# Kernel optimization log

Measured on AMD Instinct MI355X. Metric: run time of the kernel, lower is better.

## Reference

```python
import math
import jax, jax.numpy as jnp
import numpy as np

B, T, N, D = 8, 12, 512, 64
NN = 16           # neighbors per node
S_FACTOR = 5      # self.s
D_HEAD = 64       # self.d (scaling)
M_SAMPLES = int(S_FACTOR * math.log2(N))  # 45


def _ln(x):
    # LayerNorm over last dim, no affine (elementwise_affine=False)
    mu = jnp.mean(x, axis=-1, keepdims=True)
    var = jnp.var(x, axis=-1, keepdims=True)
    return (x - mu) / jnp.sqrt(var + 1e-5)


def setup_inputs() -> dict:
    key = jax.random.key(0)
    ks = jax.random.split(key, 16)
    w = lambda k, shp: jax.random.normal(k, shp, dtype=jnp.float32) * 0.05
    inp = {
        "x": jax.random.normal(ks[0], (B, T, N, D), dtype=jnp.float32),
        "adj": jax.random.randint(ks[1], (N, NN), 0, N),
        "eigvec": jax.random.normal(ks[2], (D, N, 1), dtype=jnp.float32),
        "eigvalue": jax.random.normal(ks[3], (D,), dtype=jnp.float32),
        "Wq": w(ks[4], (D, D)), "bq": jnp.zeros((D,), jnp.float32),
        "Wk": w(ks[5], (D, D)), "bk": jnp.zeros((D,), jnp.float32),
        "Wv": w(ks[6], (D, D)), "bv": jnp.zeros((D,), jnp.float32),
        "Wo": w(ks[7], (D, D)), "bo": jnp.zeros((D,), jnp.float32),
        "Wp": w(ks[8], (D, 1)), "bp": jnp.zeros((1,), jnp.float32),
        "W1": w(ks[9], (D, D)), "b1": jnp.zeros((D,), jnp.float32),
        "W2": w(ks[10], (D, D)), "b2": jnp.zeros((D,), jnp.float32),
    }
    return inp


def reference(x, adj, eigvec, eigvalue, Wq, bq, Wk, bk, Wv, bv, Wo, bo, Wp, bp, W1, b1, W2, b2):
    # x_ = x + eigvec^T.squeeze(-1) @ diag(eigvalue)  ->  [N,D] broadcast onto [B,T,N,D]
    ev = jnp.squeeze(eigvec, -1).T * eigvalue[None, :]           # [N,D]
    x_ = x + ev
    Q = x_ @ Wq + bq
    K = x_ @ Wk + bk
    V = x_ @ Wv + bv

    # adjacency-gathered GAT sampling
    K_sample = K[:, :, adj, :]                                   # [B,T,N,NN,D]
    V_sample = V[:, :, adj, :]                                   # [B,T,N,NN,D]
    qk = jnp.einsum('btnd,btnkd->btnk', Q, K_sample)             # [B,T,N,NN]
    gat = jnp.einsum('btnk,btnkd->btnd', qk, V_sample)           # [B,T,N,D]
    M = gat @ Wp[:, 0] + bp[0]                                   # [B,T,N]

    # top-k query selection (set is order-invariant downstream)
    _, M_top = jax.lax.top_k(M, M_SAMPLES)                       # [B,T,m]
    Q_red = jnp.take_along_axis(Q, M_top[..., None], axis=2)     # [B,T,m,D]

    scores = jnp.einsum('btmd,btnd->btmn', Q_red, K) / (D_HEAD ** 0.5)
    attn = jax.nn.softmax(scores, axis=-1)                       # [B,T,m,N]

    # argmax-indexed value gather: value[b,t,n] = (attn @ V)[b,t, argmax_m attn[:, n]]
    cp = jnp.argmax(attn, axis=2)                                # [B,T,N]
    av = jnp.einsum('btmn,btnd->btmd', attn, V)                  # [B,T,m,D]
    value = jnp.take_along_axis(av, cp[..., None], axis=2)       # [B,T,N,D]

    value = _ln(value @ Wo + bo + x_)
    h = jax.nn.relu(value @ W1 + b1) @ W2 + b2
    return _ln(h + value)
```

## Files before the change

### kernel.cpp

```cpp
#include <hip/hip_runtime.h>
#include <math.h>

#define Bb 8
#define Tt 12
#define Nn 512
#define Dd 64
#define NNe 16
#define MS 45
#define BT (Bb*Tt)
#define ROWS (BT*Nn)

static __device__ __forceinline__ float bcast_lane(float v, int e) {
    return __uint_as_float(__builtin_amdgcn_readlane(__float_as_uint(v), e));
}

static __device__ __forceinline__ float wave_sum(float v) {
    for (int off = 32; off; off >>= 1) v += __shfl_xor(v, off, 64);
    return v;
}
static __device__ __forceinline__ float wave_max(float v) {
    for (int off = 32; off; off >>= 1) v = fmaxf(v, __shfl_xor(v, off, 64));
    return v;
}

__global__ __launch_bounds__(256) void k_qkv(
    const float* __restrict__ x, const float* __restrict__ eigvec,
    const float* __restrict__ eigvalue,
    const float* __restrict__ Wq, const float* __restrict__ bq,
    const float* __restrict__ Wk, const float* __restrict__ bk,
    const float* __restrict__ Wv, const float* __restrict__ bv,
    float* __restrict__ xw, float* __restrict__ Qo,
    float* __restrict__ Ko, float* __restrict__ Vo)
{
    __shared__ float sWq[Dd*Dd], sWk[Dd*Dd], sWv[Dd*Dd];
    for (int i = threadIdx.x; i < Dd*Dd; i += 256) {
        sWq[i] = Wq[i]; sWk[i] = Wk[i]; sWv[i] = Wv[i];
    }
    __syncthreads();
    const int wave = threadIdx.x >> 6, lane = threadIdx.x & 63;
    const int base = (blockIdx.x * 4 + wave) * 4;
    const float evl = eigvalue[lane];

    float xs[4];
    #pragma unroll
    for (int r = 0; r < 4; ++r) {
        int row = base + r;
        int n = row & (Nn - 1);
        float v = x[(size_t)row*Dd + lane] + eigvec[lane*Nn + n] * evl;
        xs[r] = v;
        xw[(size_t)row*Dd + lane] = v;
    }
    float q[4], k[4], vv[4];
    #pragma unroll
    for (int r = 0; r < 4; ++r) { q[r] = bq[lane]; k[r] = bk[lane]; vv[r] = bv[lane]; }

    for (int e = 0; e < Dd; ++e) {
        float wq = sWq[e*Dd + lane], wk = sWk[e*Dd + lane], wv = sWv[e*Dd + lane];
        #pragma unroll
        for (int r = 0; r < 4; ++r) {
            float xe = bcast_lane(xs[r], e);
            q[r]  += xe * wq;
            k[r]  += xe * wk;
            vv[r] += xe * wv;
        }
    }
    #pragma unroll
    for (int r = 0; r < 4; ++r) {
        size_t off = (size_t)(base + r)*Dd + lane;
        Qo[off] = q[r]; Ko[off] = k[r]; Vo[off] = vv[r];
    }
}

__global__ __launch_bounds__(256) void k_gatM(
    const float* __restrict__ Q, const float* __restrict__ K,
    const float* __restrict__ V, const int* __restrict__ adj,
    const float* __restrict__ Wp, const float* __restrict__ bp,
    float* __restrict__ Mout)
{
    const int gw = blockIdx.x * 4 + (threadIdx.x >> 6);
    const int lane = threadIdx.x & 63;
    const int row = gw;
    const int bt = row >> 9, n = row & (Nn - 1);
    const float q = Q[(size_t)row*Dd + lane];
    const float* Kbt = K + (size_t)bt*Nn*Dd;
    const float* Vbt = V + (size_t)bt*Nn*Dd;
    float gat = 0.f;
    #pragma unroll 4
    for (int kk = 0; kk < NNe; ++kk) {
        int j = adj[n*NNe + kk];
        float p = wave_sum(q * Kbt[j*Dd + lane]);
        gat += p * Vbt[j*Dd + lane];
    }
    float m = wave_sum(gat * Wp[lane]);
    if (lane == 0) Mout[row] = m + bp[0];
}

__global__ __launch_bounds__(512) void k_topk(
    const float* __restrict__ Mv, int* __restrict__ Mtop)
{
    __shared__ float sv[Nn];
    __shared__ float rv[Nn];
    __shared__ int   ri[Nn];
    const int bt = blockIdx.x, t = threadIdx.x;
    sv[t] = Mv[bt*Nn + t];
    __syncthreads();
    for (int s = 0; s < MS; ++s) {
        rv[t] = sv[t]; ri[t] = t;
        __syncthreads();
        for (int off = 256; off; off >>= 1) {
            if (t < off) {
                float v2 = rv[t+off]; int i2 = ri[t+off];
                if (v2 > rv[t] || (v2 == rv[t] && i2 < ri[t])) { rv[t] = v2; ri[t] = i2; }
            }
            __syncthreads();
        }
        int w = ri[0];
        if (t == 0) Mtop[bt*MS + s] = w;
        if (t == w) sv[t] = -INFINITY;
        __syncthreads();
    }
}

__global__ __launch_bounds__(256) void k_scores(
    const float* __restrict__ Q, const float* __restrict__ K,
    const int* __restrict__ Mtop, float* __restrict__ attn)
{
    __shared__ __attribute__((aligned(16))) float sK[Dd*132];
    __shared__ __attribute__((aligned(16))) float sQ[MS*Dd];
    const int bt = blockIdx.x >> 2;
    const int n0 = (blockIdx.x & 3) * 128;
    const float* Kbt = K + (size_t)bt*Nn*Dd;
    const float* Qbt = Q + (size_t)bt*Nn*Dd;
    for (int i = threadIdx.x; i < 128*Dd; i += 256) {
        int nloc = i >> 6, e = i & 63;
        sK[e*132 + nloc] = Kbt[(n0 + nloc)*Dd + e];
    }
    for (int i = threadIdx.x; i < MS*Dd; i += 256) {
        int m = i >> 6, e = i & 63;
        sQ[i] = Qbt[(size_t)Mtop[bt*MS + m]*Dd + e];
    }
    __syncthreads();
    for (int tile = threadIdx.x; tile < 480; tile += 256) {
        const int m0 = (tile >> 5) * 3;
        const int ng = (tile & 31) * 4;
        float ax[3][4] = {};
        for (int e = 0; e < Dd; ++e) {
            const float4 kv = *reinterpret_cast<const float4*>(&sK[e*132 + ng]);
            #pragma unroll
            for (int i = 0; i < 3; ++i) {
                float qv = sQ[(m0 + i)*Dd + e];
                ax[i][0] += qv * kv.x; ax[i][1] += qv * kv.y;
                ax[i][2] += qv * kv.z; ax[i][3] += qv * kv.w;
            }
        }
        #pragma unroll
        for (int i = 0; i < 3; ++i) {
            float4 o;
            o.x = ax[i][0]*0.125f; o.y = ax[i][1]*0.125f;
            o.z = ax[i][2]*0.125f; o.w = ax[i][3]*0.125f;
            *reinterpret_cast<float4*>(
                &attn[((size_t)bt*MS + m0 + i)*Nn + n0 + ng]) = o;
        }
    }
}

__global__ __launch_bounds__(256) void k_softmax(float* __restrict__ attn)
{
    const int gw = blockIdx.x * 4 + (threadIdx.x >> 6);
    const int lane = threadIdx.x & 63;
    if (gw >= BT*MS) return;
    float* row = attn + (size_t)gw*Nn;
    float v[8];
    float mx = -INFINITY;
    #pragma unroll
    for (int i = 0; i < 8; ++i) { v[i] = row[i*64 + lane]; mx = fmaxf(mx, v[i]); }
    mx = wave_max(mx);
    float sum = 0.f;
    #pragma unroll
    for (int i = 0; i < 8; ++i) { v[i] = expf(v[i] - mx); sum += v[i]; }
    sum = wave_sum(sum);
    float inv = 1.f / sum;
    #pragma unroll
    for (int i = 0; i < 8; ++i) row[i*64 + lane] = v[i] * inv;
}

__global__ __launch_bounds__(256) void k_av(
    const float* __restrict__ attn, const float* __restrict__ V,
    float* __restrict__ av)
{
    const int gw = blockIdx.x * 4 + (threadIdx.x >> 6);
    const int lane = threadIdx.x & 63;
    if (gw >= BT*9) return;
    const int bt = gw / 9, m0 = (gw % 9) * 5;
    const float* a0 = attn + ((size_t)bt*MS + m0)*Nn;
    const float* Vbt = V + (size_t)bt*Nn*Dd;
    float acc[5] = {0,0,0,0,0};
    for (int n = 0; n < Nn; ++n) {
        float v = Vbt[n*Dd + lane];
        #pragma unroll
        for (int i = 0; i < 5; ++i) acc[i] += a0[(size_t)i*Nn + n] * v;
    }
    #pragma unroll
    for (int i = 0; i < 5; ++i)
        av[((size_t)bt*MS + m0 + i)*Dd + lane] = acc[i];
}

__global__ __launch_bounds__(256) void k_cp(
    const float* __restrict__ attn, int* __restrict__ cp)
{
    const int t = blockIdx.x * 256 + threadIdx.x;
    const int bt = t >> 9, n = t & (Nn - 1);
    const float* a = attn + (size_t)bt*MS*Nn + n;
    float best = a[0]; int bi = 0;
    for (int m = 1; m < MS; ++m) {
        float v = a[(size_t)m*Nn];
        if (v > best) { best = v; bi = m; }
    }
    cp[t] = bi;
}

__global__ __launch_bounds__(256) void k_final(
    const float* __restrict__ av, const int* __restrict__ cp,
    const float* __restrict__ xw,
    const float* __restrict__ Wo, const float* __restrict__ bo,
    const float* __restrict__ W1, const float* __restrict__ b1,
    const float* __restrict__ W2, const float* __restrict__ b2,
    float* __restrict__ out)
{
    __shared__ float sWo[Dd*Dd], sW1[Dd*Dd], sW2[Dd*Dd];
    for (int i = threadIdx.x; i < Dd*Dd; i += 256) {
        sWo[i] = Wo[i]; sW1[i] = W1[i]; sW2[i] = W2[i];
    }
    __syncthreads();
    const int wave = threadIdx.x >> 6, lane = threadIdx.x & 63;
    const int base = (blockIdx.x * 4 + wave) * 4;
    const int bt = base >> 9;

    float g[4], o[4];
    #pragma unroll
    for (int r = 0; r < 4; ++r) {
        int c = cp[base + r];
        g[r] = av[((size_t)bt*MS + c)*Dd + lane];
        o[r] = bo[lane] + xw[(size_t)(base + r)*Dd + lane];
    }
    for (int e = 0; e < Dd; ++e) {
        float w = sWo[e*Dd + lane];
        #pragma unroll
        for (int r = 0; r < 4; ++r) o[r] += bcast_lane(g[r], e) * w;
    }
    float val[4];
    #pragma unroll
    for (int r = 0; r < 4; ++r) {
        float mu = wave_sum(o[r]) * (1.f/64.f);
        float d  = o[r] - mu;
        float vs = wave_sum(d*d) * (1.f/64.f);
        val[r] = d * rsqrtf(vs + 1e-5f);
    }
    float u[4];
    #pragma unroll
    for (int r = 0; r < 4; ++r) u[r] = b1[lane];
    for (int e = 0; e < Dd; ++e) {
        float w = sW1[e*Dd + lane];
        #pragma unroll
        for (int r = 0; r < 4; ++r) u[r] += bcast_lane(val[r], e) * w;
    }
    #pragma unroll
    for (int r = 0; r < 4; ++r) u[r] = fmaxf(u[r], 0.f);
    float h[4];
    #pragma unroll
    for (int r = 0; r < 4; ++r) h[r] = b2[lane];
    for (int e = 0; e < Dd; ++e) {
        float w = sW2[e*Dd + lane];
        #pragma unroll
        for (int r = 0; r < 4; ++r) h[r] += bcast_lane(u[r], e) * w;
    }
    #pragma unroll
    for (int r = 0; r < 4; ++r) {
        float x2 = h[r] + val[r];
        float mu = wave_sum(x2) * (1.f/64.f);
        float d  = x2 - mu;
        float vs = wave_sum(d*d) * (1.f/64.f);
        out[(size_t)(base + r)*Dd + lane] = d * rsqrtf(vs + 1e-5f);
    }
}

extern "C" void kernel_launch(void* const* d_in, const int* in_sizes, int n_in,
                              void* d_out, int out_size, void* d_ws, size_t ws_size,
                              hipStream_t stream)
{
    const float* x        = (const float*)d_in[0];
    const int*   adj      = (const int*)  d_in[1];
    const float* eigvec   = (const float*)d_in[2];
    const float* eigvalue = (const float*)d_in[3];
    const float* Wq = (const float*)d_in[4],  *bq = (const float*)d_in[5];
    const float* Wk = (const float*)d_in[6],  *bk = (const float*)d_in[7];
    const float* Wv = (const float*)d_in[8],  *bv = (const float*)d_in[9];
    const float* Wo = (const float*)d_in[10], *bo = (const float*)d_in[11];
    const float* Wp = (const float*)d_in[12], *bp = (const float*)d_in[13];
    const float* W1 = (const float*)d_in[14], *b1 = (const float*)d_in[15];
    const float* W2 = (const float*)d_in[16], *b2 = (const float*)d_in[17];

    const size_t RD = (size_t)ROWS * Dd;
    float* ws   = (float*)d_ws;
    float* Q    = ws;
    float* K    = Q + RD;
    float* V    = K + RD;
    float* Mv   = V + RD;
    float* attn = Mv + ROWS;
    float* av   = attn + (size_t)BT*MS*Nn;
    int*   Mtop = (int*)(av + (size_t)BT*MS*Dd);
    int*   cp   = Mtop + BT*MS;
    float* xw   = (float*)d_out;
    float* out  = (float*)d_out;

    k_qkv   <<<ROWS/16, 256, 0, stream>>>(x, eigvec, eigvalue, Wq,bq, Wk,bk, Wv,bv, xw, Q, K, V);
    k_gatM  <<<ROWS/4,  256, 0, stream>>>(Q, K, V, adj, Wp, bp, Mv);
    k_topk  <<<BT,      512, 0, stream>>>(Mv, Mtop);
    k_scores<<<BT*4,    256, 0, stream>>>(Q, K, Mtop, attn);
    k_softmax<<<(BT*MS)/4, 256, 0, stream>>>(attn);
    k_av    <<<(BT*9)/4, 256, 0, stream>>>(attn, V, av);
    k_cp    <<<ROWS/256, 256, 0, stream>>>(attn, cp);
    k_final <<<ROWS/16, 256, 0, stream>>>(av, cp, xw, Wo,bo, W1,b1, W2,b2, out);
}
```

Baseline: 324.5 us.

## Precompute V·Wp projection, restructure GAT scoring and wave-level top-k

```diff
diff --git a/kernel.cpp b/kernel.cpp
--- a/kernel.cpp
+++ b/kernel.cpp
@@ -23,14 +23,23 @@
     return v;
 }
 
+__global__ __launch_bounds__(256) void k_evT(
+    const float* __restrict__ eigvec, const float* __restrict__ eigvalue,
+    float* __restrict__ evT)
+{
+    const int i = blockIdx.x * 256 + threadIdx.x;
+    const int d = i >> 9, n = i & (Nn - 1);
+    evT[n*Dd + d] = eigvec[i] * eigvalue[d];
+}
+
 __global__ __launch_bounds__(256) void k_qkv(
-    const float* __restrict__ x, const float* __restrict__ eigvec,
-    const float* __restrict__ eigvalue,
+    const float* __restrict__ x, const float* __restrict__ evT,
     const float* __restrict__ Wq, const float* __restrict__ bq,
     const float* __restrict__ Wk, const float* __restrict__ bk,
     const float* __restrict__ Wv, const float* __restrict__ bv,
+    const float* __restrict__ Wp,
     float* __restrict__ xw, float* __restrict__ Qo,
-    float* __restrict__ Ko, float* __restrict__ Vo)
+    float* __restrict__ Ko, float* __restrict__ Vo, float* __restrict__ pv)
 {
     __shared__ float sWq[Dd*Dd], sWk[Dd*Dd], sWv[Dd*Dd];
     for (int i = threadIdx.x; i < Dd*Dd; i += 256) {
@@ -39,14 +48,13 @@
     __syncthreads();
     const int wave = threadIdx.x >> 6, lane = threadIdx.x & 63;
     const int base = (blockIdx.x * 4 + wave) * 4;
-    const float evl = eigvalue[lane];
 
     float xs[4];
     #pragma unroll
     for (int r = 0; r < 4; ++r) {
         int row = base + r;
         int n = row & (Nn - 1);
-        float v = x[(size_t)row*Dd + lane] + eigvec[lane*Nn + n] * evl;
+        float v = x[(size_t)row*Dd + lane] + evT[n*Dd + lane];
         xs[r] = v;
         xw[(size_t)row*Dd + lane] = v;
     }
@@ -64,60 +72,83 @@
             vv[r] += xe * wv;
         }
     }
+    const float wp = Wp[lane];
     #pragma unroll
     for (int r = 0; r < 4; ++r) {
         size_t off = (size_t)(base + r)*Dd + lane;
         Qo[off] = q[r]; Ko[off] = k[r]; Vo[off] = vv[r];
-    }
-}
-
-__global__ __launch_bounds__(256) void k_gatM(
+        float p = wave_sum(vv[r] * wp);
+        if (lane == 0) pv[base + r] = p;
+    }
+}
+
+__global__ __launch_bounds__(256) void k_M(
     const float* __restrict__ Q, const float* __restrict__ K,
-    const float* __restrict__ V, const int* __restrict__ adj,
-    const float* __restrict__ Wp, const float* __restrict__ bp,
-    float* __restrict__ Mout)
-{
-    const int gw = blockIdx.x * 4 + (threadIdx.x >> 6);
+    const int* __restrict__ adj, const float* __restrict__ pv,
+    const float* __restrict__ bp, float* __restrict__ Mout)
+{
+    __shared__ __attribute__((aligned(16))) float sK[Nn*Dd];
+    const int bt = blockIdx.x >> 1;
+    const int half = blockIdx.x & 1;
+
+    const float4* Ksrc = reinterpret_cast<const float4*>(K + (size_t)bt*Nn*Dd);
+    float4* sK4 = reinterpret_cast<float4*>(sK);
+    for (int i4 = threadIdx.x; i4 < Nn*16; i4 += 256) {
+        int nn = i4 >> 4, e4 = i4 & 15;
+        sK4[(nn << 4) | (e4 ^ (nn & 15))] = Ksrc[i4];
+    }
+    __syncthreads();
+
+    const int n = half*256 + threadIdx.x;
+    float4 q4[16];
+    const float4* Qr = reinterpret_cast<const float4*>(Q + ((size_t)bt*Nn + n)*Dd);
+    #pragma unroll
+    for (int i = 0; i < 16; ++i) q4[i] = Qr[i];
+
+    const float* pvbt = pv + (size_t)bt*Nn;
+    float m = bp[0];
+    #pragma unroll 1
+    for (int k = 0; k < NNe; ++k) {
+        const int j = adj[(n << 4) + k];
+        const float4* kr = sK4 + ((size_t)j << 4);
+        const int sw = j & 15;
+        float dot = 0.f;
+        #pragma unroll
+        for (int e4 = 0; e4 < 16; ++e4) {
+            float4 kv = kr[e4 ^ sw];
+            dot += q4[e4].x*kv.x + q4[e4].y*kv.y + q4[e4].z*kv.z + q4[e4].w*kv.w;
+        }
+        m += dot * pvbt[j];
+    }
+    Mout[bt*Nn + n] = m;
+}
+
+__global__ __launch_bounds__(256) void k_topk(
+    const float* __restrict__ Mv, int* __restrict__ Mtop)
+{
+    const int bt = blockIdx.x * 4 + (threadIdx.x >> 6);
     const int lane = threadIdx.x & 63;
-    const int row = gw;
-    const int bt = row >> 9, n = row & (Nn - 1);
-    const float q = Q[(size_t)row*Dd + lane];
-    const float* Kbt = K + (size_t)bt*Nn*Dd;
-    const float* Vbt = V + (size_t)bt*Nn*Dd;
-    float gat = 0.f;
-    #pragma unroll 4
-    for (int kk = 0; kk < NNe; ++kk) {
-        int j = adj[n*NNe + kk];
-        float p = wave_sum(q * Kbt[j*Dd + lane]);
-        gat += p * Vbt[j*Dd + lane];
-    }
-    float m = wave_sum(gat * Wp[lane]);
-    if (lane == 0) Mout[row] = m + bp[0];
-}
-
-__global__ __launch_bounds__(512) void k_topk(
-    const float* __restrict__ Mv, int* __restrict__ Mtop)
-{
-    __shared__ float sv[Nn];
-    __shared__ float rv[Nn];
-    __shared__ int   ri[Nn];
-    const int bt = blockIdx.x, t = threadIdx.x;
-    sv[t] = Mv[bt*Nn + t];
-    __syncthreads();
+    float v[8];
+    #pragma unroll
+    for (int i = 0; i < 8; ++i) v[i] = Mv[bt*Nn + i*64 + lane];
     for (int s = 0; s < MS; ++s) {
-        rv[t] = sv[t]; ri[t] = t;
-        __syncthreads();
-        for (int off = 256; off; off >>= 1) {
-            if (t < off) {
-                float v2 = rv[t+off]; int i2 = ri[t+off];
-                if (v2 > rv[t] || (v2 == rv[t] && i2 < ri[t])) { rv[t] = v2; ri[t] = i2; }
-            }
-            __syncthreads();
-        }
-        int w = ri[0];
-        if (t == 0) Mtop[bt*MS + s] = w;
-        if (t == w) sv[t] = -INFINITY;
-        __syncthreads();
+        float bv = v[0]; int bn = lane;
+        #pragma unroll
+        for (int i = 1; i < 8; ++i) {
+            int nn = i*64 + lane;
+            if (v[i] > bv) { bv = v[i]; bn = nn; }
+        }
+        for (int off = 32; off; off >>= 1) {
+            float ov = __shfl_xor(bv, off, 64);
+            int   on = __shfl_xor(bn, off, 64);
+            if (ov > bv || (ov == bv && on < bn)) { bv = ov; bn = on; }
+        }
+        if (lane == 0) Mtop[bt*MS + s] = bn;
+        const int wl = bn & 63, wi = bn >> 6;
+        if (lane == wl) {
+            #pragma unroll
+            for (int i = 0; i < 8; ++i) if (i == wi) v[i] = -INFINITY;
+        }
     }
 }
 
@@ -308,14 +339,17 @@
     float* Mv   = V + RD;
     float* attn = Mv + ROWS;
     float* av   = attn + (size_t)BT*MS*Nn;
-    int*   Mtop = (int*)(av + (size_t)BT*MS*Dd);
+    float* pv   = av + (size_t)BT*MS*Dd;
+    float* evT  = pv + ROWS;
+    int*   Mtop = (int*)(evT + Nn*Dd);
     int*   cp   = Mtop + BT*MS;
     float* xw   = (float*)d_out;
     float* out  = (float*)d_out;
 
-    k_qkv   <<<ROWS/16, 256, 0, stream>>>(x, eigvec, eigvalue, Wq,bq, Wk,bk, Wv,bv, xw, Q, K, V);
-    k_gatM  <<<ROWS/4,  256, 0, stream>>>(Q, K, V, adj, Wp, bp, Mv);
-    k_topk  <<<BT,      512, 0, stream>>>(Mv, Mtop);
+    k_evT   <<<(Dd*Nn)/256, 256, 0, stream>>>(eigvec, eigvalue, evT);
+    k_qkv   <<<ROWS/16, 256, 0, stream>>>(x, evT, Wq,bq, Wk,bk, Wv,bv, Wp, xw, Q, K, V, pv);
+    k_M     <<<BT*2,    256, 0, stream>>>(Q, K, adj, pv, bp, Mv);
+    k_topk  <<<BT/4,    256, 0, stream>>>(Mv, Mtop);
     k_scores<<<BT*4,    256, 0, stream>>>(Q, K, Mtop, attn);
     k_softmax<<<(BT*MS)/4, 256, 0, stream>>>(attn);
     k_av    <<<(BT*9)/4, 256, 0, stream>>>(attn, V, av);
```

New measurement: 273.3 us. -15.8%, faster.
